# Kernel tuning notes

Hardware: AMD Instinct MI355X
Metric: run time of the kernel (lower is better)

Reference implementation:

```python
import jax, jax.numpy as jnp
import numpy as np

B, T, C, H = 2, 2048, 1024, 16
D = C // H  # head dim = 64
NEG_MIN = jnp.finfo(jnp.float32).min


def setup_inputs() -> dict:
    key = jax.random.key(0)
    ks = jax.random.split(key, 5)
    std = 0.02
    return {
        "x": jax.random.normal(ks[0], (B, T, C), dtype=jnp.float32),
        "Wq": std * jax.random.normal(ks[1], (C, C), dtype=jnp.float32),
        "bq": jnp.zeros((C,), dtype=jnp.float32),
        "Wk": std * jax.random.normal(ks[2], (C, C), dtype=jnp.float32),
        "bk": jnp.zeros((C,), dtype=jnp.float32),
        "Wv": std * jax.random.normal(ks[3], (C, C), dtype=jnp.float32),
        "bv": jnp.zeros((C,), dtype=jnp.float32),
        "Wo": (std / np.sqrt(24.0)) * jax.random.normal(ks[4], (C, C), dtype=jnp.float32),
        "bo": jnp.zeros((C,), dtype=jnp.float32),
    }


def reference(x, Wq, bq, Wk, bk, Wv, bv, Wo, bo):
    # QKV projections -> (B, H, T, D)
    def proj(W, b):
        return (x @ W + b).reshape(B, T, H, D).transpose(0, 2, 1, 3)

    q = proj(Wq, bq)
    k = proj(Wk, bk)
    v = proj(Wv, bv)

    # full scores (B, H, T, T), causal mask, softmax
    attn = jnp.einsum("bhqd,bhkd->bhqk", q, k) / jnp.sqrt(jnp.float32(D))
    mask = jnp.tril(jnp.ones((T, T), dtype=bool))[None, None]
    attn = jnp.where(mask, attn, NEG_MIN)
    scores = jax.nn.softmax(attn, axis=-1)

    out = jnp.einsum("bhqk,bhkd->bhqd", scores, v)
    out = out.transpose(0, 2, 1, 3).reshape(B, T, C)
    return out @ Wo + bo
```

## Files before the change

kernel.cpp:

```cpp
#include <hip/hip_runtime.h>
#include <stdint.h>
#include <stddef.h>


#define B_SZ 2
#define T_SZ 2048
#define C_SZ 1024
#define H_SZ 16
#define D_SZ 64
#define M_SZ (B_SZ * T_SZ)
#define BHTD (B_SZ * H_SZ * T_SZ * D_SZ)
#define CC (C_SZ * C_SZ)

typedef __attribute__((ext_vector_type(8))) __bf16 bf16x8;
typedef __attribute__((ext_vector_type(4))) float f32x4;
typedef __attribute__((ext_vector_type(16))) float f32x16;

__device__ __forceinline__ unsigned short f2bf(float f) {
    union { float f; unsigned u; } v; v.f = f;
    v.u += 0x7fffu + ((v.u >> 16) & 1u);
    return (unsigned short)(v.u >> 16);
}

__device__ __forceinline__ unsigned pkbf(float lo, float hi_) {
    union { unsigned u; __bf16 h[2]; } r;
    r.h[0] = (__bf16)lo; r.h[1] = (__bf16)hi_;
    return r.u;
}

__device__ __forceinline__ void load_lds16(const unsigned short* g, unsigned short* l) {
    __builtin_amdgcn_global_load_lds(
        (const __attribute__((address_space(1))) void*)g,
        (__attribute__((address_space(3))) void*)l, 16, 0, 0);
}


__global__ void cvt_x_kernel(const float4* __restrict__ in, ushort4* __restrict__ out, int n4) {
    int stride = gridDim.x * blockDim.x;
    for (int i = blockIdx.x * blockDim.x + threadIdx.x; i < n4; i += stride) {
        float4 v = in[i];
        ushort4 o;
        o.x = f2bf(v.x); o.y = f2bf(v.y); o.z = f2bf(v.z); o.w = f2bf(v.w);
        out[i] = o;
    }
}

__global__ __launch_bounds__(256) void transpose_cvt_kernel(
    const float* __restrict__ W0, const float* __restrict__ W1,
    const float* __restrict__ W2, const float* __restrict__ W3,
    unsigned short* __restrict__ T0, unsigned short* __restrict__ T1,
    unsigned short* __restrict__ T2, unsigned short* __restrict__ T3)
{
    __shared__ float tile[32][33];
    const float* W; unsigned short* Wt;
    switch (blockIdx.z) {
        case 0: W = W0; Wt = T0; break;
        case 1: W = W1; Wt = T1; break;
        case 2: W = W2; Wt = T2; break;
        default: W = W3; Wt = T3; break;
    }
    const int tx = threadIdx.x, ty = threadIdx.y;
    const int n0 = blockIdx.x * 32, k0 = blockIdx.y * 32;
    #pragma unroll
    for (int i = 0; i < 4; i++)
        tile[ty + i * 8][tx] = W[(size_t)(k0 + ty + i * 8) * C_SZ + n0 + tx];
    __syncthreads();
    #pragma unroll
    for (int i = 0; i < 4; i++)
        Wt[(size_t)(n0 + ty + i * 8) * C_SZ + k0 + tx] = f2bf(tile[tx][ty + i * 8]);
}

__global__ __launch_bounds__(256) void vt_kernel(
    const unsigned short* __restrict__ V, unsigned short* __restrict__ Vt)
{
    __shared__ unsigned short tile[32][33];
    const int bh = blockIdx.z;
    const int t0 = blockIdx.x * 32, d0 = blockIdx.y * 32;
    const unsigned short* src = V + (size_t)bh * T_SZ * D_SZ;
    unsigned short* dst = Vt + (size_t)bh * T_SZ * D_SZ;
    const int tx = threadIdx.x, ty = threadIdx.y;
    #pragma unroll
    for (int i = 0; i < 4; i++)
        tile[ty + i * 8][tx] = src[(size_t)(t0 + ty + i * 8) * D_SZ + d0 + tx];
    __syncthreads();
    #pragma unroll
    for (int i = 0; i < 4; i++)
        dst[(size_t)(d0 + ty + i * 8) * T_SZ + t0 + tx] = tile[tx][ty + i * 8];
}


__device__ __forceinline__ void gemm_tile_core(
    const unsigned short* __restrict__ A,
    const unsigned short* __restrict__ Bt,
    unsigned short* As, unsigned short* Bs,
    int m0, int n0, f32x4 acc[4][4])
{
    const int tid = threadIdx.x;
    const int lane = tid & 63;
    const int w = tid >> 6;
    const int l15 = lane & 15, lg = lane >> 4;
    const int wr = (w >> 1) * 64, wc = (w & 1) * 64;

    const unsigned short* Ag0 = A + (size_t)(m0 + (tid >> 2)) * C_SZ + (tid & 3) * 8;
    const unsigned short* Ag1 = Ag0 + (size_t)64 * C_SZ;
    const unsigned short* Bg0 = Bt + (size_t)(n0 + (tid >> 2)) * C_SZ + (tid & 3) * 8;
    const unsigned short* Bg1 = Bg0 + (size_t)64 * C_SZ;
    unsigned short* As0 = As + w * 512;
    unsigned short* As1 = As + 2048 + w * 512;
    unsigned short* Bs0 = Bs + w * 512;
    unsigned short* Bs1 = Bs + 2048 + w * 512;

    for (int k0 = 0; k0 < C_SZ; k0 += 32) {
        load_lds16(Ag0 + k0, As0);
        load_lds16(Ag1 + k0, As1);
        load_lds16(Bg0 + k0, Bs0);
        load_lds16(Bg1 + k0, Bs1);
        __syncthreads();
        bf16x8 af[4], bfv[4];
        const bf16x8* Ap = (const bf16x8*)As;
        const bf16x8* Bp = (const bf16x8*)Bs;
        #pragma unroll
        for (int m = 0; m < 4; m++) af[m] = Ap[(wr + m * 16 + l15) * 4 + lg];
        #pragma unroll
        for (int n = 0; n < 4; n++) bfv[n] = Bp[(wc + n * 16 + l15) * 4 + lg];
        #pragma unroll
        for (int m = 0; m < 4; m++)
            #pragma unroll
            for (int n = 0; n < 4; n++)
                acc[m][n] = __builtin_amdgcn_mfma_f32_16x16x32_bf16(af[m], bfv[n], acc[m][n], 0, 0, 0);
        __syncthreads();
    }
}

__global__ __launch_bounds__(256) void gemm_qkv_kernel(
    const unsigned short* __restrict__ A,
    const unsigned short* __restrict__ WtBase,
    const float* __restrict__ bq, const float* __restrict__ bk, const float* __restrict__ bv,
    unsigned short* __restrict__ QKV, unsigned short* __restrict__ Vtmp)
{
    __shared__ unsigned short As[4096], Bs[4096];
    const int z = blockIdx.z;
    const unsigned short* Bt = WtBase + (size_t)z * CC;
    const float* bias = (z == 0) ? bq : (z == 1) ? bk : bv;
    const float scale = (z == 0) ? 0.18033688011112042f : 1.0f;
    unsigned short* Out = (z == 2) ? Vtmp : QKV + (size_t)z * BHTD;

    f32x4 acc[4][4];
    f32x4 zero4 = {0.f, 0.f, 0.f, 0.f};
    #pragma unroll
    for (int m = 0; m < 4; m++)
        #pragma unroll
        for (int n = 0; n < 4; n++) acc[m][n] = zero4;

    const int m0 = blockIdx.y * 128, n0 = blockIdx.x * 128;
    gemm_tile_core(A, Bt, As, Bs, m0, n0, acc);

    const int lane = threadIdx.x & 63;
    const int w = threadIdx.x >> 6;
    const int l15 = lane & 15, lg = lane >> 4;
    const int wr = (w >> 1) * 64, wc = (w & 1) * 64;
    #pragma unroll
    for (int n = 0; n < 4; n++) {
        const int col = n0 + wc + n * 16 + l15;
        const float bias_v = bias[col];
        const int h = col >> 6, d = col & 63;
        #pragma unroll
        for (int m = 0; m < 4; m++) {
            #pragma unroll
            for (int j = 0; j < 4; j++) {
                const int row = m0 + wr + m * 16 + lg * 4 + j;
                const int b = row >> 11, t = row & (T_SZ - 1);
                Out[(((size_t)(b * H_SZ + h)) * T_SZ + t) * D_SZ + d] =
                    f2bf((acc[m][n][j] + bias_v) * scale);
            }
        }
    }
}

__global__ __launch_bounds__(256) void gemm_out_kernel(
    const unsigned short* __restrict__ A,
    const unsigned short* __restrict__ Bt,
    const float* __restrict__ bo,
    float* __restrict__ Out)
{
    __shared__ unsigned short As[4096], Bs[4096];
    f32x4 acc[4][4];
    f32x4 zero4 = {0.f, 0.f, 0.f, 0.f};
    #pragma unroll
    for (int m = 0; m < 4; m++)
        #pragma unroll
        for (int n = 0; n < 4; n++) acc[m][n] = zero4;

    const int m0 = blockIdx.y * 128, n0 = blockIdx.x * 128;
    gemm_tile_core(A, Bt, As, Bs, m0, n0, acc);

    const int lane = threadIdx.x & 63;
    const int w = threadIdx.x >> 6;
    const int l15 = lane & 15, lg = lane >> 4;
    const int wr = (w >> 1) * 64, wc = (w & 1) * 64;
    #pragma unroll
    for (int n = 0; n < 4; n++) {
        const int col = n0 + wc + n * 16 + l15;
        const float bias_v = bo[col];
        #pragma unroll
        for (int m = 0; m < 4; m++) {
            #pragma unroll
            for (int j = 0; j < 4; j++) {
                const int row = m0 + wr + m * 16 + lg * 4 + j;
                Out[(size_t)row * C_SZ + col] = acc[m][n][j] + bias_v;
            }
        }
    }
}

__global__ __launch_bounds__(256) void attn_fwd_kernel(
    const unsigned short* __restrict__ Q,
    const unsigned short* __restrict__ K,
    const unsigned short* __restrict__ Vt,
    unsigned short* __restrict__ O)
{
    const int idx = blockIdx.x;
    const int qt = (idx < 256) ? (15 - (idx >> 5)) : ((idx - 256) >> 5);
    const int bh = idx & 31;
    const int w = threadIdx.x >> 6;
    const int lane = threadIdx.x & 63;
    const int l31 = lane & 31, hi = lane >> 5;
    const int qw = qt * 128 + 32 * w;

    const unsigned short* Qh = Q + (size_t)bh * T_SZ * D_SZ;
    const unsigned short* Kh = K + (size_t)bh * T_SZ * D_SZ;
    const unsigned short* Vh = Vt + (size_t)bh * T_SZ * D_SZ;

    __shared__ __align__(16) unsigned short smem[16384];

    const int c0 = w * 64 + lane;
    const int row0 = c0 >> 3;
    const int sw0 = (c0 & 7) ^ (row0 & 7);
    const int koff0 = row0 * 64 + sw0 * 8;
    const int voff0 = row0 * T_SZ + sw0 * 8;
    const int ldsb0 = w * 512;

    bf16x8 qf[4];
    #pragma unroll
    for (int j = 0; j < 4; j++)
        qf[j] = *(const bf16x8*)&Qh[(size_t)(qw + l31) * D_SZ + j * 16 + 8 * hi];

    f32x16 acc[2];
    #pragma unroll
    for (int r = 0; r < 16; r++) { acc[0][r] = 0.f; acc[1][r] = 0.f; }
    float mrun = -3.0e38f, lrun = 0.f;

    const int tlast = (qw + 31) >> 6;
    const int ntb = 2 * qt + 2;
    const int qrow = qw + l31;
    const int swl = l31 & 7;

    load_lds16(Kh + koff0, smem + ldsb0);
    load_lds16(Kh + koff0 + 2048, smem + 2048 + ldsb0);
    load_lds16(Vh + voff0, smem + 4096 + ldsb0);
    load_lds16(Vh + voff0 + 32 * T_SZ, smem + 6144 + ldsb0);

    for (int tt = 0; tt < ntb; ++tt) {
        if (tt + 1 < ntb) {
            unsigned short* Bd = smem + ((tt + 1) & 1) * 8192;
            const unsigned short* Kt = Kh + (size_t)(tt + 1) * 64 * D_SZ;
            const unsigned short* Vtt = Vh + (tt + 1) * 64;
            load_lds16(Kt + koff0, Bd + ldsb0);
            load_lds16(Kt + koff0 + 2048, Bd + 2048 + ldsb0);
            load_lds16(Vtt + voff0, Bd + 4096 + ldsb0);
            load_lds16(Vtt + voff0 + 32 * T_SZ, Bd + 6144 + ldsb0);
            asm volatile("s_waitcnt vmcnt(4)" ::: "memory");
        } else {
            asm volatile("s_waitcnt vmcnt(0)" ::: "memory");
        }
        __builtin_amdgcn_s_barrier();

        if (tt <= tlast) {
            const unsigned short* Ks = smem + (tt & 1) * 8192;
            const unsigned short* Vs = Ks + 4096;
            const int k0 = tt * 64;

            f32x16 s[2];
            #pragma unroll
            for (int kb = 0; kb < 2; ++kb) {
                bf16x8 kf[4];
                #pragma unroll
                for (int j = 0; j < 4; ++j) {
                    const int ch = (j * 2 + hi) ^ swl;
                    kf[j] = *(const bf16x8*)&Ks[(kb * 32 + l31) * 64 + ch * 8];
                }
                f32x16 sc;
                #pragma unroll
                for (int r = 0; r < 16; r++) sc[r] = 0.f;
                #pragma unroll
                for (int j = 0; j < 4; ++j)
                    sc = __builtin_amdgcn_mfma_f32_32x32x16_bf16(kf[j], qf[j], sc, 0, 0, 0);
                s[kb] = sc;
            }

            if (k0 + 63 > qw) {
                #pragma unroll
                for (int kb = 0; kb < 2; ++kb)
                    #pragma unroll
                    for (int r = 0; r < 16; ++r) {
                        const int kv = k0 + kb * 32 + (r & 3) + 8 * (r >> 2) + 4 * hi;
                        s[kb][r] = (kv > qrow) ? -3.0e38f : s[kb][r];
                    }
            }

            float pm = s[0][0];
            #pragma unroll
            for (int r = 1; r < 16; r++) pm = fmaxf(pm, s[0][r]);
            #pragma unroll
            for (int r = 0; r < 16; r++) pm = fmaxf(pm, s[1][r]);
            pm = fmaxf(pm, __shfl_xor(pm, 32));

            if (!__all(pm <= mrun + 8.0f)) {
                const float mnew = fmaxf(mrun, pm);
                const float al = exp2f(mrun - mnew);
                lrun *= al;
                #pragma unroll
                for (int r = 0; r < 16; r++) { acc[0][r] *= al; acc[1][r] *= al; }
                mrun = mnew;
            }

            float ps = 0.f;
            #pragma unroll
            for (int kb = 0; kb < 2; ++kb)
                #pragma unroll
                for (int r = 0; r < 16; r++) { s[kb][r] = exp2f(s[kb][r] - mrun); ps += s[kb][r]; }
            ps += __shfl_xor(ps, 32);
            lrun += ps;

            bf16x8 pf[2][2];
            #pragma unroll
            for (int kb = 0; kb < 2; ++kb) {
                #pragma unroll
                for (int ksl = 0; ksl < 2; ++ksl) {
                    unsigned a0 = pkbf(s[kb][8 * ksl + 0], s[kb][8 * ksl + 1]);
                    unsigned a1 = pkbf(s[kb][8 * ksl + 2], s[kb][8 * ksl + 3]);
                    unsigned b0 = pkbf(s[kb][8 * ksl + 4], s[kb][8 * ksl + 5]);
                    unsigned b1 = pkbf(s[kb][8 * ksl + 6], s[kb][8 * ksl + 7]);
                    asm volatile("v_permlane32_swap_b32 %0, %1" : "+v"(a0), "+v"(b0));
                    asm volatile("v_permlane32_swap_b32 %0, %1" : "+v"(a1), "+v"(b1));
                    union { unsigned u[4]; bf16x8 v; } fr;
                    fr.u[0] = a0; fr.u[1] = a1; fr.u[2] = b0; fr.u[3] = b1;
                    pf[kb][ksl] = fr.v;
                }
            }

            #pragma unroll
            for (int dt = 0; dt < 2; ++dt)
                #pragma unroll
                for (int kb = 0; kb < 2; ++kb)
                    #pragma unroll
                    for (int ksl = 0; ksl < 2; ++ksl) {
                        const int ks = kb * 2 + ksl;
                        const int ch = (ks * 2 + hi) ^ swl;
                        const bf16x8 vf = *(const bf16x8*)&Vs[(dt * 32 + l31) * 64 + ch * 8];
                        acc[dt] = __builtin_amdgcn_mfma_f32_32x32x16_bf16(vf, pf[kb][ksl], acc[dt], 0, 0, 0);
                    }
        }
        __builtin_amdgcn_s_barrier();
    }

    unsigned short* ot = smem + w * 2304;
    const float inv = 1.0f / lrun;
    #pragma unroll
    for (int g = 0; g < 4; g++) {
        ushort4 wa, wb;
        wa.x = f2bf(acc[0][4 * g + 0] * inv); wa.y = f2bf(acc[0][4 * g + 1] * inv);
        wa.z = f2bf(acc[0][4 * g + 2] * inv); wa.w = f2bf(acc[0][4 * g + 3] * inv);
        wb.x = f2bf(acc[1][4 * g + 0] * inv); wb.y = f2bf(acc[1][4 * g + 1] * inv);
        wb.z = f2bf(acc[1][4 * g + 2] * inv); wb.w = f2bf(acc[1][4 * g + 3] * inv);
        *(ushort4*)&ot[l31 * 72 + 8 * g + 4 * hi] = wa;
        *(ushort4*)&ot[l31 * 72 + 32 + 8 * g + 4 * hi] = wb;
    }
    const int b = bh >> 4, h = bh & 15;
    #pragma unroll
    for (int pss = 0; pss < 4; pss++) {
        const int q = pss * 8 + (lane >> 3);
        const uint4 val = *(const uint4*)&ot[q * 72 + (lane & 7) * 8];
        *(uint4*)&O[((size_t)(b * T_SZ + qw + q)) * C_SZ + h * D_SZ + (lane & 7) * 8] = val;
    }
}


extern "C" void kernel_launch(void* const* d_in, const int* in_sizes, int n_in,
                              void* d_out, int out_size, void* d_ws, size_t ws_size,
                              hipStream_t stream)
{
    const float* x  = (const float*)d_in[0];
    const float* Wq = (const float*)d_in[1];
    const float* bq = (const float*)d_in[2];
    const float* Wk = (const float*)d_in[3];
    const float* bk = (const float*)d_in[4];
    const float* Wv = (const float*)d_in[5];
    const float* bv = (const float*)d_in[6];
    const float* Wo = (const float*)d_in[7];
    const float* bo = (const float*)d_in[8];

    uint8_t* ws = (uint8_t*)d_ws;
    unsigned short* XB   = (unsigned short*)(ws);
    unsigned short* WT   = (unsigned short*)(ws + (8u  << 20));
    unsigned short* QKV  = (unsigned short*)(ws + (16u << 20));
    unsigned short* Vtmp = (unsigned short*)(ws + (40u << 20));

    cvt_x_kernel<<<2048, 256, 0, stream>>>((const float4*)x, (ushort4*)XB, M_SZ * C_SZ / 4);
    transpose_cvt_kernel<<<dim3(32, 32, 4), dim3(32, 8), 0, stream>>>(
        Wq, Wk, Wv, Wo, WT, WT + CC, WT + 2 * (size_t)CC, WT + 3 * (size_t)CC);
    gemm_qkv_kernel<<<dim3(8, 32, 3), 256, 0, stream>>>(XB, WT, bq, bk, bv, QKV, Vtmp);
    vt_kernel<<<dim3(64, 2, 32), dim3(32, 8), 0, stream>>>(Vtmp, QKV + 2 * (size_t)BHTD);
    attn_fwd_kernel<<<512, 256, 0, stream>>>(
        QKV, QKV + BHTD, QKV + 2 * (size_t)BHTD, Vtmp);
    gemm_out_kernel<<<dim3(8, 32), 256, 0, stream>>>(Vtmp, WT + 3 * (size_t)CC, bo, (float*)d_out);
}
```

Measured before the change: 131.8 us.

## Enlarge attention KV tile to 128 keys and use tree reductions

```diff
diff --git a/kernel.cpp b/kernel.cpp
--- a/kernel.cpp
+++ b/kernel.cpp
@@ -231,13 +231,15 @@
     const unsigned short* Kh = K + (size_t)bh * T_SZ * D_SZ;
     const unsigned short* Vh = Vt + (size_t)bh * T_SZ * D_SZ;
 
-    __shared__ __align__(16) unsigned short smem[16384];
+    __shared__ __align__(16) unsigned short smem[32768];
 
     const int c0 = w * 64 + lane;
-    const int row0 = c0 >> 3;
-    const int sw0 = (c0 & 7) ^ (row0 & 7);
-    const int koff0 = row0 * 64 + sw0 * 8;
-    const int voff0 = row0 * T_SZ + sw0 * 8;
+    const int krow0 = c0 >> 3;
+    const int ksw0 = (c0 & 7) ^ (krow0 & 7);
+    const int koff0 = krow0 * 64 + ksw0 * 8;
+    const int vrow0 = c0 >> 4;
+    const int vsw0 = (c0 & 15) ^ (vrow0 & 15);
+    const int voff0 = vrow0 * T_SZ + vsw0 * 8;
     const int ldsb0 = w * 512;
 
     bf16x8 qf[4];
@@ -250,43 +252,47 @@
     for (int r = 0; r < 16; r++) { acc[0][r] = 0.f; acc[1][r] = 0.f; }
     float mrun = -3.0e38f, lrun = 0.f;
 
-    const int tlast = (qw + 31) >> 6;
-    const int ntb = 2 * qt + 2;
+    const int ntb = qt + 1;
     const int qrow = qw + l31;
-    const int swl = l31 & 7;
-
-    load_lds16(Kh + koff0, smem + ldsb0);
-    load_lds16(Kh + koff0 + 2048, smem + 2048 + ldsb0);
-    load_lds16(Vh + voff0, smem + 4096 + ldsb0);
-    load_lds16(Vh + voff0 + 32 * T_SZ, smem + 6144 + ldsb0);
+    const int kswl = l31 & 7;
+    const int vswl = l31 & 15;
+
+    #pragma unroll
+    for (int ii = 0; ii < 4; ii++)
+        load_lds16(Kh + koff0 + ii * 2048, smem + ldsb0 + ii * 2048);
+    #pragma unroll
+    for (int ii = 0; ii < 4; ii++)
+        load_lds16(Vh + voff0 + ii * 16 * T_SZ, smem + 8192 + ldsb0 + ii * 2048);
 
     for (int tt = 0; tt < ntb; ++tt) {
         if (tt + 1 < ntb) {
-            unsigned short* Bd = smem + ((tt + 1) & 1) * 8192;
-            const unsigned short* Kt = Kh + (size_t)(tt + 1) * 64 * D_SZ;
-            const unsigned short* Vtt = Vh + (tt + 1) * 64;
-            load_lds16(Kt + koff0, Bd + ldsb0);
-            load_lds16(Kt + koff0 + 2048, Bd + 2048 + ldsb0);
-            load_lds16(Vtt + voff0, Bd + 4096 + ldsb0);
-            load_lds16(Vtt + voff0 + 32 * T_SZ, Bd + 6144 + ldsb0);
-            asm volatile("s_waitcnt vmcnt(4)" ::: "memory");
+            unsigned short* Bd = smem + ((tt + 1) & 1) * 16384;
+            const unsigned short* Kt = Kh + (size_t)(tt + 1) * 128 * D_SZ;
+            const unsigned short* Vtt = Vh + (tt + 1) * 128;
+            #pragma unroll
+            for (int ii = 0; ii < 4; ii++)
+                load_lds16(Kt + koff0 + ii * 2048, Bd + ldsb0 + ii * 2048);
+            #pragma unroll
+            for (int ii = 0; ii < 4; ii++)
+                load_lds16(Vtt + voff0 + ii * 16 * T_SZ, Bd + 8192 + ldsb0 + ii * 2048);
+            asm volatile("s_waitcnt vmcnt(8)" ::: "memory");
         } else {
             asm volatile("s_waitcnt vmcnt(0)" ::: "memory");
         }
         __builtin_amdgcn_s_barrier();
 
-        if (tt <= tlast) {
-            const unsigned short* Ks = smem + (tt & 1) * 8192;
-            const unsigned short* Vs = Ks + 4096;
-            const int k0 = tt * 64;
-
-            f32x16 s[2];
-            #pragma unroll
-            for (int kb = 0; kb < 2; ++kb) {
+        {
+            const unsigned short* Ks = smem + (tt & 1) * 16384;
+            const unsigned short* Vs = Ks + 8192;
+            const int k0 = tt * 128;
+
+            f32x16 s[4];
+            #pragma unroll
+            for (int kb = 0; kb < 4; ++kb) {
                 bf16x8 kf[4];
                 #pragma unroll
                 for (int j = 0; j < 4; ++j) {
-                    const int ch = (j * 2 + hi) ^ swl;
+                    const int ch = (j * 2 + hi) ^ kswl;
                     kf[j] = *(const bf16x8*)&Ks[(kb * 32 + l31) * 64 + ch * 8];
                 }
                 f32x16 sc;
@@ -298,9 +304,9 @@
                 s[kb] = sc;
             }
 
-            if (k0 + 63 > qw) {
-                #pragma unroll
-                for (int kb = 0; kb < 2; ++kb)
+            if (tt == ntb - 1) {
+                #pragma unroll
+                for (int kb = 0; kb < 4; ++kb)
                     #pragma unroll
                     for (int r = 0; r < 16; ++r) {
                         const int kv = k0 + kb * 32 + (r & 3) + 8 * (r >> 2) + 4 * hi;
@@ -308,12 +314,16 @@
                     }
             }
 
-            float pm = s[0][0];
-            #pragma unroll
-            for (int r = 1; r < 16; r++) pm = fmaxf(pm, s[0][r]);
-            #pragma unroll
-            for (int r = 0; r < 16; r++) pm = fmaxf(pm, s[1][r]);
-            pm = fmaxf(pm, __shfl_xor(pm, 32));
+            float t32[32];
+            #pragma unroll
+            for (int i = 0; i < 32; i++)
+                t32[i] = fmaxf(s[(2 * i) >> 4][(2 * i) & 15], s[(2 * i + 1) >> 4][(2 * i + 1) & 15]);
+            #pragma unroll
+            for (int st = 16; st >= 1; st >>= 1)
+                #pragma unroll
+                for (int i = 0; i < st; i++)
+                    t32[i] = fmaxf(t32[i], t32[i + st]);
+            const float pm = fmaxf(t32[0], __shfl_xor(t32[0], 32));
 
             if (!__all(pm <= mrun + 8.0f)) {
                 const float mnew = fmaxf(mrun, pm);
@@ -324,17 +334,24 @@
                 mrun = mnew;
             }
 
-            float ps = 0.f;
-            #pragma unroll
-            for (int kb = 0; kb < 2; ++kb)
-                #pragma unroll
-                for (int r = 0; r < 16; r++) { s[kb][r] = exp2f(s[kb][r] - mrun); ps += s[kb][r]; }
-            ps += __shfl_xor(ps, 32);
-            lrun += ps;
-
-            bf16x8 pf[2][2];
-            #pragma unroll
-            for (int kb = 0; kb < 2; ++kb) {
+            #pragma unroll
+            for (int kb = 0; kb < 4; ++kb)
+                #pragma unroll
+                for (int r = 0; r < 16; r++) s[kb][r] = exp2f(s[kb][r] - mrun);
+            float a32[32];
+            #pragma unroll
+            for (int i = 0; i < 32; i++)
+                a32[i] = s[(2 * i) >> 4][(2 * i) & 15] + s[(2 * i + 1) >> 4][(2 * i + 1) & 15];
+            #pragma unroll
+            for (int st = 16; st >= 1; st >>= 1)
+                #pragma unroll
+                for (int i = 0; i < st; i++)
+                    a32[i] += a32[i + st];
+            lrun += a32[0] + __shfl_xor(a32[0], 32);
+
+            bf16x8 pf[4][2];
+            #pragma unroll
+            for (int kb = 0; kb < 4; ++kb) {
                 #pragma unroll
                 for (int ksl = 0; ksl < 2; ++ksl) {
                     unsigned a0 = pkbf(s[kb][8 * ksl + 0], s[kb][8 * ksl + 1]);
@@ -352,12 +369,12 @@
             #pragma unroll
             for (int dt = 0; dt < 2; ++dt)
                 #pragma unroll
-                for (int kb = 0; kb < 2; ++kb)
+                for (int kb = 0; kb < 4; ++kb)
                     #pragma unroll
                     for (int ksl = 0; ksl < 2; ++ksl) {
                         const int ks = kb * 2 + ksl;
-                        const int ch = (ks * 2 + hi) ^ swl;
-                        const bf16x8 vf = *(const bf16x8*)&Vs[(dt * 32 + l31) * 64 + ch * 8];
+                        const int ch = (ks * 2 + hi) ^ vswl;
+                        const bf16x8 vf = *(const bf16x8*)&Vs[(dt * 32 + l31) * 128 + ch * 8];
                         acc[dt] = __builtin_amdgcn_mfma_f32_32x32x16_bf16(vf, pf[kb][ksl], acc[dt], 0, 0, 0);
                     }
         }
```

Measured after the change: 145.4 us. 1.1x slower.
